# Optimization experiments

Hardware: AMD Instinct MI355X
Metric: run time of the kernel (lower is better)

The kernel has to match this reference:

```python
import jax, jax.numpy as jnp
import numpy as np
from jax import lax

SPARSITY = 0.5  # args.sparsity: fraction of weights KEPT


def get_subnet(scores, k):
    """GetSubnet.forward: sort |scores|, zero lowest (1-k) fraction, one elsewhere."""
    sa = jnp.abs(scores)
    n = sa.size
    j = int((1.0 - k) * n)  # static: number of entries zeroed
    idx = jnp.argsort(sa.ravel())  # ascending, matches torch .sort()
    mask = jnp.zeros((n,), dtype=sa.dtype).at[idx[j:]].set(1.0)
    return mask.reshape(scores.shape)


def masked_conv(x, w, s, b, stride):
    m = get_subnet(s, SPARSITY)
    y = lax.conv_general_dilated(
        x, w * m, window_strides=(stride, stride), padding=((1, 1), (1, 1)),
        dimension_numbers=('NCHW', 'OIHW', 'NCHW'))
    return y + b[None, :, None, None]


def setup_inputs() -> dict:
    key = jax.random.key(0)
    ks = jax.random.split(key, 16)
    def rn(k, shape, scale):
        return jax.random.normal(k, shape, dtype=jnp.float32) * scale
    return {
        'x':   rn(ks[0], (64, 3, 64, 64), 1.0),
        'w1':  rn(ks[1], (128, 3, 3, 3), 0.2),   's1': rn(ks[2], (128, 3, 3, 3), 1.0),   'b1': rn(ks[3], (128,), 0.01),
        'w2':  rn(ks[4], (256, 128, 3, 3), 0.05), 's2': rn(ks[5], (256, 128, 3, 3), 1.0), 'b2': rn(ks[6], (256,), 0.01),
        'w3':  rn(ks[7], (512, 256, 3, 3), 0.03), 's3': rn(ks[8], (512, 256, 3, 3), 1.0), 'b3': rn(ks[9], (512,), 0.01),
        'fw1': rn(ks[10], (1024, 512), 0.05),     'fs1': rn(ks[11], (1024, 512), 1.0),    'fb1': rn(ks[12], (1024,), 0.01),
        'fw2': rn(ks[13], (10, 1024), 0.05),      'fs2': rn(ks[14], (10, 1024), 1.0),     'fb2': rn(ks[15], (10,), 0.01),
    }


def reference(x, w1, s1, b1, w2, s2, b2, w3, s3, b3, fw1, fs1, fb1, fw2, fs2, fb2):
    h = jax.nn.relu(masked_conv(x, w1, s1, b1, stride=1))   # [64,128,64,64]
    h = jax.nn.relu(masked_conv(h, w2, s2, b2, stride=2))   # [64,256,32,32]
    h = jax.nn.relu(masked_conv(h, w3, s3, b3, stride=2))   # [64,512,16,16]
    h = h.mean(axis=(2, 3))                                 # [64,512] global avg pool
    m1 = get_subnet(fs1, SPARSITY)
    h = jax.nn.relu(h @ (fw1 * m1).T + fb1)                 # [64,1024]
    m2 = get_subnet(fs2, SPARSITY)
    return h @ (fw2 * m2).T + fb2                           # [64,10]
```

## Files before the change

### kernel.cpp

```cpp
#include <hip/hip_runtime.h>
#include <stdint.h>


typedef __attribute__((ext_vector_type(8))) short short8;
typedef __attribute__((ext_vector_type(4))) short short4v;
typedef __attribute__((ext_vector_type(4))) float floatx4;
typedef __attribute__((ext_vector_type(4))) int int4v;

__device__ __forceinline__ unsigned short f2bf(float f) {
    unsigned u = __float_as_uint(f);
    u += 0x7fffu + ((u >> 16) & 1u);
    return (unsigned short)(u >> 16);
}

__device__ __forceinline__ short8 gload16(const unsigned short* p) {
    int4v d;
    asm volatile("global_load_dwordx4 %0, %1, off" : "=v"(d) : "v"(p));
    union { int4v i; short8 s; } u;
    u.i = d;
    return u.s;
}

constexpr unsigned CUM0 = 3456u;
constexpr unsigned CUM1 = 298368u;
constexpr unsigned CUM2 = 1478016u;
constexpr unsigned CUM3 = 2002304u;
constexpr unsigned STOT = 2012544u;
constexpr int NBH = 512;

__device__ __forceinline__ int find_tensor(unsigned idx, unsigned& li) {
    if (idx < CUM0) { li = idx;        return 0; }
    if (idx < CUM1) { li = idx - CUM0; return 1; }
    if (idx < CUM2) { li = idx - CUM1; return 2; }
    if (idx < CUM3) { li = idx - CUM2; return 3; }
    li = idx - CUM3; return 4;
}

__global__ __launch_bounds__(256) void hist11(const float* __restrict__ s0,
                                              const float* __restrict__ s1,
                                              const float* __restrict__ s2,
                                              const float* __restrict__ s3,
                                              const float* __restrict__ s4,
                                              const unsigned* __restrict__ P,
                                              unsigned* __restrict__ ghist, int pass) {
    __shared__ unsigned lh[10240];
    const int tid = threadIdx.x;
    const int NB = (pass == 2) ? 512 : 2048;
    for (int i = tid; i < NB * 5; i += 256) lh[i] = 0;
    __syncthreads();

    unsigned pref[5];
    #pragma unroll
    for (int t = 0; t < 5; t++) pref[t] = pass ? P[t] : 0u;
    const int fsh = (pass == 1) ? 20 : 9;

    for (unsigned idx = blockIdx.x * 256u + tid; idx < STOT; idx += NBH * 256u) {
        unsigned li; int t = find_tensor(idx, li);
        const float* sp = t == 0 ? s0 : t == 1 ? s1 : t == 2 ? s2 : t == 3 ? s3 : s4;
        unsigned key = __float_as_uint(sp[li]) & 0x7fffffffu;
        bool ok = (pass == 0) || ((key >> fsh) == pref[t]);
        if (ok) {
            unsigned bin = (pass == 0) ? (key >> 20)
                         : (pass == 1) ? ((key >> 9) & 2047u)
                                       : (key & 511u);
            atomicAdd(&lh[(unsigned)t * NB + bin], 1u);
        }
    }
    __syncthreads();
    const int goff = (pass == 0) ? 0 : (pass == 1) ? 10240 : 20480;
    for (int i = tid; i < NB * 5; i += 256) {
        unsigned v = lh[i];
        if (v) atomicAdd(&ghist[goff + i], v);
    }
}

__global__ __launch_bounds__(256) void find11(const unsigned* __restrict__ ghist,
                                              unsigned* __restrict__ P,
                                              unsigned* __restrict__ targ, int pass) {
    const int t = blockIdx.x;
    const int tid = threadIdx.x;
    const int NB = (pass == 2) ? 512 : 2048;
    const int goff = (pass == 0) ? 0 : (pass == 1) ? 10240 : 20480;
    const int seg = NB / 256;
    __shared__ unsigned bins[2048];
    __shared__ unsigned part[256];
    for (int i = tid; i < NB; i += 256) bins[i] = ghist[goff + t * NB + i];
    __syncthreads();
    unsigned s = 0;
    for (int j = 0; j < seg; j++) s += bins[tid * seg + j];
    part[tid] = s;
    __syncthreads();
    if (tid == 0) {
        unsigned n = t == 0 ? 3456u : t == 1 ? 294912u : t == 2 ? 1179648u
                   : t == 3 ? 524288u : 10240u;
        unsigned target = (pass == 0) ? (n >> 1) : targ[t];
        unsigned cum = 0; int q = 0;
        for (; q < 256; q++) { unsigned c = part[q]; if (cum + c > target) break; cum += c; }
        int b = q * seg;
        for (;; b++) { unsigned c = bins[b]; if (cum + c > target) break; cum += c; }
        targ[t] = target - cum;
        if (pass == 0)      P[t] = (unsigned)b;
        else if (pass == 1) P[t] = (P[t] << 11) | (unsigned)b;
        else                P[t] = (P[t] << 9) | (unsigned)b;
    }
}

__global__ void mask_reorder(const float* __restrict__ w0, const float* __restrict__ w1,
                             const float* __restrict__ w2, const float* __restrict__ w3,
                             const float* __restrict__ w4,
                             const float* __restrict__ s0, const float* __restrict__ s1,
                             const float* __restrict__ s2, const float* __restrict__ s3,
                             const float* __restrict__ s4,
                             const unsigned* __restrict__ T,
                             float* __restrict__ wm1,
                             unsigned short* __restrict__ A2,
                             unsigned short* __restrict__ A3,
                             float* __restrict__ fwm1, float* __restrict__ fwm2,
                             float* __restrict__ pooled) {
    unsigned idx = blockIdx.x * 256u + threadIdx.x;
    if (idx >= STOT) return;
    if (idx < 32768u) pooled[idx] = 0.f;
    unsigned li; int t = find_tensor(idx, li);
    const float* sp = t == 0 ? s0 : t == 1 ? s1 : t == 2 ? s2 : t == 3 ? s3 : s4;
    const float* wp = t == 0 ? w0 : t == 1 ? w1 : t == 2 ? w2 : t == 3 ? w3 : w4;
    unsigned key = __float_as_uint(sp[li]) & 0x7fffffffu;
    float val = (key >= T[t]) ? wp[li] : 0.f;
    if (t == 0) {
        wm1[li] = val;
    } else if (t == 1) {
        unsigned k = li / 1152u, r = li - k * 1152u;
        unsigned c = r / 9u, e = r - c * 9u;
        A2[((size_t)e * 256u + k) * 128u + c] = f2bf(val);
    } else if (t == 2) {
        unsigned k = li / 2304u, r = li - k * 2304u;
        unsigned c = r / 9u, e = r - c * 9u;
        A3[((size_t)e * 512u + k) * 256u + c] = f2bf(val);
    } else if (t == 3) {
        fwm1[li] = val;
    } else {
        fwm2[li] = val;
    }
}

template <int C, int H, int W, int K, int TX, int TY, int KT>
__global__ __launch_bounds__(TX* TY) void conv_direct(const float* __restrict__ in,
                                                      const float* __restrict__ wm,
                                                      const float* __restrict__ bias,
                                                      unsigned short* __restrict__ out) {
    constexpr int TILW = TX * 2, TILH = TY * 2;
    constexpr int ITW = TILW + 2, ITH = TILH + 2;
    constexpr int NTHREADS = TX * TY;
    constexpr int NLOAD = (ITH * ITW + NTHREADS - 1) / NTHREADS;
    constexpr int KG = K / KT;

    __shared__ float sIn[ITH * ITW];
    __shared__ float sW[9 * KT];

    const int tid = threadIdx.x;
    const int tx = tid % TX, ty = tid / TX;
    const int kg = blockIdx.z % KG, n = blockIdx.z / KG;
    const int ox0 = blockIdx.x * TILW, oy0 = blockIdx.y * TILH;
    const int ix0 = ox0 - 1, iy0 = oy0 - 1;

    const float* inN = in + (size_t)n * C * H * W;
    const float* wkg = wm + (size_t)kg * KT * C * 9;

    int goff[NLOAD];
    #pragma unroll
    for (int i = 0; i < NLOAD; i++) {
        int idx = tid + i * NTHREADS;
        if (idx < ITH * ITW) {
            int r = idx / ITW, col = idx % ITW;
            int gy = iy0 + r, gx = ix0 + col;
            goff[i] = (gy >= 0 && gy < H && gx >= 0 && gx < W) ? (gy * W + gx) : -1;
        } else goff[i] = -2;
    }

    float acc[2][2][KT];
    #pragma unroll
    for (int py = 0; py < 2; py++)
        #pragma unroll
        for (int px = 0; px < 2; px++)
            #pragma unroll
            for (int j = 0; j < KT; j++) acc[py][px][j] = 0.f;

    for (int c = 0; c < C; c++) {
        const float* inC = inN + (size_t)c * H * W;
        #pragma unroll
        for (int i = 0; i < NLOAD; i++) {
            int g = goff[i];
            if (g >= -1) sIn[tid + i * NTHREADS] = (g >= 0) ? inC[g] : 0.f;
        }
        for (int i = tid; i < 9 * KT; i += NTHREADS) {
            int e = i / KT, j = i % KT;
            sW[i] = wkg[j * C * 9 + c * 9 + e];
        }
        __syncthreads();

        float vin[4][4];
        const float* base = &sIn[(ty * 2) * ITW + tx * 2];
        #pragma unroll
        for (int r = 0; r < 4; r++)
            #pragma unroll
            for (int cc = 0; cc < 4; cc++) vin[r][cc] = base[r * ITW + cc];

        #pragma unroll
        for (int e = 0; e < 9; e++) {
            const int dy = e / 3, dx = e % 3;
            #pragma unroll
            for (int j = 0; j < KT; j++) {
                float wv = sW[e * KT + j];
                #pragma unroll
                for (int py = 0; py < 2; py++)
                    #pragma unroll
                    for (int px = 0; px < 2; px++)
                        acc[py][px][j] = fmaf(vin[py + dy][px + dx], wv, acc[py][px][j]);
            }
        }
        __syncthreads();
    }

    float bj[KT];
    #pragma unroll
    for (int j = 0; j < KT; j++) bj[j] = bias[kg * KT + j];
    #pragma unroll
    for (int py = 0; py < 2; py++)
        #pragma unroll
        for (int px = 0; px < 2; px++) {
            int oy = oy0 + ty * 2 + py, ox = ox0 + tx * 2 + px;
            short8 v;
            #pragma unroll
            for (int j = 0; j < KT; j++) {
                float t = acc[py][px][j] + bj[j];
                v[j] = (short)f2bf(t > 0.f ? t : 0.f);
            }
            *(short8*)(out + ((size_t)(n * H + oy) * W + ox) * K + kg * KT) = v;
        }
}

template <int C, int H, int W, int KOUT, int NPIX, bool POOL, bool SWAPYZ>
__global__ __launch_bounds__(256, 3) void conv_mfma(const unsigned short* __restrict__ in,
                                                    const unsigned short* __restrict__ A,
                                                    const float* __restrict__ bias,
                                                    void* __restrict__ outv) {
    constexpr int OH = H / 2, OW = W / 2;
    constexpr int PR = NPIX / OW;
    constexpr int FN = NPIX / 16;
    constexpr int RH = 2 * PR + 1;
    constexpr int IW = W + 1;
    constexpr int NC = C / 32;
    constexpr int PSTR = 40;
    constexpr int NSLOT = RH * IW * 4;
    constexpr int SLMAX = (NSLOT + 255) / 256;

    __shared__ unsigned short sIn[RH * IW * PSTR];

    const int tid = threadIdx.x;
    const int lane = tid & 63;
    const int wv = tid >> 6;
    const int l15 = lane & 15;
    const int quad = lane >> 4;
    const int pt = blockIdx.x;
    const int kb = SWAPYZ ? blockIdx.z : blockIdx.y;
    const int n  = SWAPYZ ? blockIdx.y : blockIdx.z;
    const int k0 = kb * 128;
    const int oy0 = pt * PR;
    const int g0y = 2 * oy0 - 1;
    const int mw = wv * 32;

    int goff[SLMAX], slds[SLMAX];
    #pragma unroll
    for (int i = 0; i < SLMAX; i++) {
        int s = tid + i * 256;
        if (s < NSLOT) {
            int q = s & 3, pix = s >> 2;
            int ix = pix % IW, iy = pix / IW;
            int gy = g0y + iy, gx = ix - 1;
            slds[i] = pix * PSTR + q * 8;
            goff[i] = (gy >= 0 && gy < H && gx >= 0) ? ((gy * W + gx) * C + q * 8) : -1;
        } else { goff[i] = -2; slds[i] = 0; }
    }

    int pB[FN];
    #pragma unroll
    for (int fn = 0; fn < FN; fn++) {
        int p = fn * 16 + l15;
        int oyl = p / OW, oxl = p % OW;
        pB[fn] = (oyl * 2 * IW + oxl * 2) * PSTR + quad * 8;
    }

    const unsigned short* inN = in + (size_t)n * H * W * C;

    floatx4 acc[2][FN];
    #pragma unroll
    for (int fm = 0; fm < 2; fm++)
        #pragma unroll
        for (int fn = 0; fn < FN; fn++) acc[fm][fn] = (floatx4){0.f, 0.f, 0.f, 0.f};

    #pragma unroll 1
    for (int cc = 0; cc < NC; cc++) {
        const int cof = cc * 32;
        const unsigned short* Abase = A + (size_t)(k0 + mw + l15) * C + cof + quad * 8;
        const size_t estr = (size_t)KOUT * C;

        __syncthreads();

        short8 af[9][2];
        #pragma unroll
        for (int e = 0; e < 9; e++) {
            af[e][0] = gload16(Abase + (size_t)e * estr);
            af[e][1] = gload16(Abase + (size_t)e * estr + 16 * C);
        }

        #pragma unroll
        for (int i = 0; i < SLMAX; i++) {
            int g = goff[i];
            if (g >= 0) {
                *(short8*)&sIn[slds[i]] = *(const short8*)(inN + g + cof);
            } else if (g == -1 && cc == 0) {
                *(short8*)&sIn[slds[i]] = (short8){0, 0, 0, 0, 0, 0, 0, 0};
            }
        }
        __syncthreads();
        asm volatile("s_waitcnt vmcnt(0)" ::: "memory");
        __builtin_amdgcn_sched_barrier(0);

        #pragma unroll
        for (int e = 0; e < 9; e++) {
            const int dy = e / 3, dx = e - dy * 3;
            const int boff = (dy * IW + dx) * PSTR;
            short8 bfr[FN];
            #pragma unroll
            for (int fn = 0; fn < FN; fn++)
                bfr[fn] = *(const short8*)&sIn[pB[fn] + boff];
            #pragma unroll
            for (int fn = 0; fn < FN; fn++) {
                acc[0][fn] = __builtin_amdgcn_mfma_f32_16x16x32_bf16(af[e][0], bfr[fn], acc[0][fn], 0, 0, 0);
                acc[1][fn] = __builtin_amdgcn_mfma_f32_16x16x32_bf16(af[e][1], bfr[fn], acc[1][fn], 0, 0, 0);
            }
        }
    }

    if (!POOL) {
        unsigned short* out = (unsigned short*)outv;
        #pragma unroll
        for (int fm = 0; fm < 2; fm++) {
            const int k4 = k0 + mw + fm * 16 + quad * 4;
            float b0 = bias[k4], b1 = bias[k4 + 1], b2 = bias[k4 + 2], b3 = bias[k4 + 3];
            #pragma unroll
            for (int fn = 0; fn < FN; fn++) {
                int p = fn * 16 + l15;
                int oy = oy0 + p / OW, ox = p % OW;
                float v0 = acc[fm][fn][0] + b0, v1 = acc[fm][fn][1] + b1;
                float v2 = acc[fm][fn][2] + b2, v3 = acc[fm][fn][3] + b3;
                short4v v;
                v[0] = (short)f2bf(v0 > 0.f ? v0 : 0.f);
                v[1] = (short)f2bf(v1 > 0.f ? v1 : 0.f);
                v[2] = (short)f2bf(v2 > 0.f ? v2 : 0.f);
                v[3] = (short)f2bf(v3 > 0.f ? v3 : 0.f);
                *(short4v*)(out + ((size_t)(n * OH + oy) * OW + ox) * KOUT + k4) = v;
            }
        }
    } else {
        float* out = (float*)outv;
        #pragma unroll
        for (int fm = 0; fm < 2; fm++) {
            #pragma unroll
            for (int reg = 0; reg < 4; reg++) {
                int k = k0 + mw + fm * 16 + quad * 4 + reg;
                float bv = bias[k];
                float s = 0.f;
                #pragma unroll
                for (int fn = 0; fn < FN; fn++) {
                    float v = acc[fm][fn][reg] + bv;
                    s += v > 0.f ? v : 0.f;
                }
                s += __shfl_xor(s, 1); s += __shfl_xor(s, 2);
                s += __shfl_xor(s, 4); s += __shfl_xor(s, 8);
                if (l15 == 0) atomicAdd(&out[n * KOUT + k], s * (1.0f / (OH * OW)));
            }
        }
    }
}

__global__ void fc1_kernel(const float* __restrict__ pooled, const float* __restrict__ w,
                           const float* __restrict__ b, float* __restrict__ out) {
    int t = blockIdx.x * 256 + threadIdx.x;
    int o = t & 1023, n = t >> 10;
    const float4* w4 = (const float4*)(w + (size_t)o * 512);
    const float4* p4 = (const float4*)(pooled + (size_t)n * 512);
    float acc = 0.f;
    for (int i = 0; i < 128; i++) {
        float4 a = p4[i], ww = w4[i];
        acc += a.x * ww.x + a.y * ww.y + a.z * ww.z + a.w * ww.w;
    }
    acc += b[o];
    out[t] = acc > 0.f ? acc : 0.f;
}

__global__ void fc2_kernel(const float* __restrict__ h, const float* __restrict__ w,
                           const float* __restrict__ b, float* __restrict__ out) {
    int n = blockIdx.x, tid = threadIdx.x;
    __shared__ float redw[40];
    const float4* h4 = (const float4*)(h + (size_t)n * 1024);
    float4 a = h4[tid];
    for (int o = 0; o < 10; o++) {
        const float4* w4 = (const float4*)(w + (size_t)o * 1024);
        float4 ww = w4[tid];
        float v = a.x * ww.x + a.y * ww.y + a.z * ww.z + a.w * ww.w;
        for (int off = 32; off > 0; off >>= 1) v += __shfl_down(v, off);
        if ((tid & 63) == 0) redw[o * 4 + (tid >> 6)] = v;
    }
    __syncthreads();
    if (tid < 10) {
        float s = redw[tid * 4] + redw[tid * 4 + 1] + redw[tid * 4 + 2] + redw[tid * 4 + 3] + b[tid];
        out[n * 10 + tid] = s;
    }
}

extern "C" void kernel_launch(void* const* d_in, const int* in_sizes, int n_in,
                              void* d_out, int out_size, void* d_ws, size_t ws_size,
                              hipStream_t stream) {
    const float* x   = (const float*)d_in[0];
    const float* w1  = (const float*)d_in[1];
    const float* s1  = (const float*)d_in[2];
    const float* b1  = (const float*)d_in[3];
    const float* w2  = (const float*)d_in[4];
    const float* s2  = (const float*)d_in[5];
    const float* b2  = (const float*)d_in[6];
    const float* w3  = (const float*)d_in[7];
    const float* s3  = (const float*)d_in[8];
    const float* b3  = (const float*)d_in[9];
    const float* fw1 = (const float*)d_in[10];
    const float* fs1 = (const float*)d_in[11];
    const float* fb1 = (const float*)d_in[12];
    const float* fw2 = (const float*)d_in[13];
    const float* fs2 = (const float*)d_in[14];
    const float* fb2 = (const float*)d_in[15];
    float* out = (float*)d_out;

    char* ws = (char*)d_ws;
    size_t off = 0;
    auto alloc = [&](size_t bytes) -> char* {
        char* p = ws + off;
        off = (off + bytes + 255) & ~(size_t)255;
        return p;
    };
    unsigned* ghist = (unsigned*)alloc(23040ull * 4);
    unsigned* P     = (unsigned*)alloc(64);
    unsigned* targ  = (unsigned*)alloc(64);
    float* wm1  = (float*)alloc(3456ull * 4);
    float* fwm1 = (float*)alloc(524288ull * 4);
    float* fwm2 = (float*)alloc(10240ull * 4);
    unsigned short* A2 = (unsigned short*)alloc(294912ull * 2);
    unsigned short* A3 = (unsigned short*)alloc(1179648ull * 2);
    unsigned short* h1 = (unsigned short*)alloc(33554432ull * 2);
    unsigned short* h2 = (unsigned short*)alloc(16777216ull * 2);
    float* pooled = (float*)alloc(32768ull * 4);
    float* fc1h   = (float*)alloc(65536ull * 4);
    if (off > ws_size) return;

    (void)hipMemsetAsync(ghist, 0, 23040ull * 4, stream);

    for (int pass = 0; pass < 3; pass++) {
        hist11<<<NBH, 256, 0, stream>>>(s1, s2, s3, fs1, fs2, P, ghist, pass);
        find11<<<5, 256, 0, stream>>>(ghist, P, targ, pass);
    }
    int gs = (STOT + 255) / 256;
    mask_reorder<<<gs, 256, 0, stream>>>(w1, w2, w3, fw1, fw2, s1, s2, s3, fs1, fs2, P,
                                         wm1, A2, A3, fwm1, fwm2, pooled);

    conv_direct<3, 64, 64, 128, 16, 16, 8>
        <<<dim3(2, 2, 64 * 16), 256, 0, stream>>>(x, wm1, b1, h1);
    conv_mfma<128, 64, 64, 256, 64, false, false>
        <<<dim3(16, 2, 64), 256, 0, stream>>>(h1, A2, b2, h2);
    conv_mfma<256, 32, 32, 512, 64, true, true>
        <<<dim3(4, 64, 4), 256, 0, stream>>>(h2, A3, b3, pooled);

    fc1_kernel<<<256, 256, 0, stream>>>(pooled, fwm1, fb1, fc1h);
    fc2_kernel<<<64, 256, 0, stream>>>(fc1h, fwm2, fb2, out);
}
```

Baseline: 459.0 us.

## Double-buffer conv input staging via direct global-to-LDS loads with swizzled layout

Replaces the register-staged input tile copy in the MFMA conv kernels with global_load_lds direct-to-LDS loads into a double-buffered shared array, prefetching the next channel chunk while the current one is computed. The LDS layout changes from a padded per-pixel stride to a channel-quad-major layout with an XOR swizzle to avoid bank conflicts, and out-of-bounds pixels read from a zeroed guard buffer in the workspace. Weight fragment loads become plain loads instead of volatile asm. The cost is doubled LDS use, which may lower occupancy, and extra index arithmetic per LDS read.

```diff
diff --git a/kernel.cpp b/kernel.cpp
--- a/kernel.cpp
+++ b/kernel.cpp
@@ -5,7 +5,6 @@
 typedef __attribute__((ext_vector_type(8))) short short8;
 typedef __attribute__((ext_vector_type(4))) short short4v;
 typedef __attribute__((ext_vector_type(4))) float floatx4;
-typedef __attribute__((ext_vector_type(4))) int int4v;
 
 __device__ __forceinline__ unsigned short f2bf(float f) {
     unsigned u = __float_as_uint(f);
@@ -13,12 +12,11 @@
     return (unsigned short)(u >> 16);
 }
 
-__device__ __forceinline__ short8 gload16(const unsigned short* p) {
-    int4v d;
-    asm volatile("global_load_dwordx4 %0, %1, off" : "=v"(d) : "v"(p));
-    union { int4v i; short8 s; } u;
-    u.i = d;
-    return u.s;
+__device__ __forceinline__ void stage16(const unsigned short* g, unsigned short* l) {
+    __builtin_amdgcn_global_load_lds(
+        (const __attribute__((address_space(1))) unsigned int*)(const void*)g,
+        (__attribute__((address_space(3))) unsigned int*)(void*)l,
+        16, 0, 0);
 }
 
 constexpr unsigned CUM0 = 3456u;
@@ -242,6 +240,7 @@
 __global__ __launch_bounds__(256, 3) void conv_mfma(const unsigned short* __restrict__ in,
                                                     const unsigned short* __restrict__ A,
                                                     const float* __restrict__ bias,
+                                                    const unsigned short* __restrict__ zg,
                                                     void* __restrict__ outv) {
     constexpr int OH = H / 2, OW = W / 2;
     constexpr int PR = NPIX / OW;
@@ -249,11 +248,13 @@
     constexpr int RH = 2 * PR + 1;
     constexpr int IW = W + 1;
     constexpr int NC = C / 32;
-    constexpr int PSTR = 40;
-    constexpr int NSLOT = RH * IW * 4;
+    constexpr int NPT = RH * IW;
+    constexpr int NPTP = (NPT + 7) & ~7;
+    constexpr int NSLOT = 4 * NPTP;
     constexpr int SLMAX = (NSLOT + 255) / 256;
-
-    __shared__ unsigned short sIn[RH * IW * PSTR];
+    constexpr int SLOTS_PAD = SLMAX * 256;
+
+    __shared__ unsigned short sIn[2][SLOTS_PAD * 8];
 
     const int tid = threadIdx.x;
     const int lane = tid & 63;
@@ -268,25 +269,25 @@
     const int g0y = 2 * oy0 - 1;
     const int mw = wv * 32;
 
-    int goff[SLMAX], slds[SLMAX];
+    int goff[SLMAX];
     #pragma unroll
     for (int i = 0; i < SLMAX; i++) {
         int s = tid + i * 256;
-        if (s < NSLOT) {
-            int q = s & 3, pix = s >> 2;
-            int ix = pix % IW, iy = pix / IW;
-            int gy = g0y + iy, gx = ix - 1;
-            slds[i] = pix * PSTR + q * 8;
-            goff[i] = (gy >= 0 && gy < H && gx >= 0) ? ((gy * W + gx) * C + q * 8) : -1;
-        } else { goff[i] = -2; slds[i] = 0; }
-    }
-
-    int pB[FN];
+        int q = s / NPTP;
+        int pix = s - q * NPTP;
+        int pl = pix ^ ((pix >> 3) & 7);
+        int iy = pl / IW, ix = pl - iy * IW;
+        int gy = g0y + iy, gx = ix - 1;
+        bool ok = (q < 4) && (pl < NPT) && (gy >= 0) && (gy < H) && (gx >= 0);
+        goff[i] = ok ? ((gy * W + gx) * C + q * 8) : -1;
+    }
+
+    int pL[FN];
     #pragma unroll
     for (int fn = 0; fn < FN; fn++) {
         int p = fn * 16 + l15;
         int oyl = p / OW, oxl = p % OW;
-        pB[fn] = (oyl * 2 * IW + oxl * 2) * PSTR + quad * 8;
+        pL[fn] = oyl * 2 * IW + oxl * 2;
     }
 
     const unsigned short* inN = in + (size_t)n * H * W * C;
@@ -296,49 +297,60 @@
     for (int fm = 0; fm < 2; fm++)
         #pragma unroll
         for (int fn = 0; fn < FN; fn++) acc[fm][fn] = (floatx4){0.f, 0.f, 0.f, 0.f};
+
+    auto stage_chunk = [&](unsigned short* sbuf, int cc) {
+        const int cof = cc * 32;
+        #pragma unroll
+        for (int i = 0; i < SLMAX; i++) {
+            const unsigned short* src = (goff[i] >= 0) ? (inN + goff[i] + cof) : zg;
+            stage16(src, sbuf + (size_t)(tid + i * 256) * 8);
+        }
+    };
+
+    const size_t estr = (size_t)KOUT * C;
+
+    stage_chunk(&sIn[0][0], 0);
 
     #pragma unroll 1
     for (int cc = 0; cc < NC; cc++) {
-        const int cof = cc * 32;
-        const unsigned short* Abase = A + (size_t)(k0 + mw + l15) * C + cof + quad * 8;
-        const size_t estr = (size_t)KOUT * C;
-
-        __syncthreads();
-
+        const int cur = cc & 1;
+        const unsigned short* sb = &sIn[cur][0];
+
+        if (cc + 1 < NC) {
+            stage_chunk(&sIn[cur ^ 1][0], cc + 1);
+            asm volatile("s_waitcnt vmcnt(%0)" :: "n"(SLMAX) : "memory");
+        } else {
+            asm volatile("s_waitcnt vmcnt(0)" ::: "memory");
+        }
+        __builtin_amdgcn_s_barrier();
+        __builtin_amdgcn_sched_barrier(0);
+
+        const unsigned short* Abase = A + (size_t)(k0 + mw + l15) * C + cc * 32 + quad * 8;
         short8 af[9][2];
         #pragma unroll
         for (int e = 0; e < 9; e++) {
-            af[e][0] = gload16(Abase + (size_t)e * estr);
-            af[e][1] = gload16(Abase + (size_t)e * estr + 16 * C);
-        }
-
-        #pragma unroll
-        for (int i = 0; i < SLMAX; i++) {
-            int g = goff[i];
-            if (g >= 0) {
-                *(short8*)&sIn[slds[i]] = *(const short8*)(inN + g + cof);
-            } else if (g == -1 && cc == 0) {
-                *(short8*)&sIn[slds[i]] = (short8){0, 0, 0, 0, 0, 0, 0, 0};
-            }
-        }
-        __syncthreads();
-        asm volatile("s_waitcnt vmcnt(0)" ::: "memory");
-        __builtin_amdgcn_sched_barrier(0);
+            af[e][0] = *(const short8*)(Abase + (size_t)e * estr);
+            af[e][1] = *(const short8*)(Abase + (size_t)e * estr + 16 * C);
+        }
 
         #pragma unroll
         for (int e = 0; e < 9; e++) {
             const int dy = e / 3, dx = e - dy * 3;
-            const int boff = (dy * IW + dx) * PSTR;
+            const int tof = dy * IW + dx;
             short8 bfr[FN];
             #pragma unroll
-            for (int fn = 0; fn < FN; fn++)
-                bfr[fn] = *(const short8*)&sIn[pB[fn] + boff];
+            for (int fn = 0; fn < FN; fn++) {
+                int p = pL[fn] + tof;
+                int pl = p ^ ((p >> 3) & 7);
+                bfr[fn] = *(const short8*)(sb + ((size_t)quad * NPTP + pl) * 8);
+            }
             #pragma unroll
             for (int fn = 0; fn < FN; fn++) {
                 acc[0][fn] = __builtin_amdgcn_mfma_f32_16x16x32_bf16(af[e][0], bfr[fn], acc[0][fn], 0, 0, 0);
                 acc[1][fn] = __builtin_amdgcn_mfma_f32_16x16x32_bf16(af[e][1], bfr[fn], acc[1][fn], 0, 0, 0);
             }
         }
+        __builtin_amdgcn_s_barrier();
     }
 
     if (!POOL) {
@@ -447,6 +459,7 @@
         return p;
     };
     unsigned* ghist = (unsigned*)alloc(23040ull * 4);
+    unsigned short* zguard = (unsigned short*)alloc(256);
     unsigned* P     = (unsigned*)alloc(64);
     unsigned* targ  = (unsigned*)alloc(64);
     float* wm1  = (float*)alloc(3456ull * 4);
@@ -460,7 +473,7 @@
     float* fc1h   = (float*)alloc(65536ull * 4);
     if (off > ws_size) return;
 
-    (void)hipMemsetAsync(ghist, 0, 23040ull * 4, stream);
+    (void)hipMemsetAsync(ghist, 0, 23040ull * 4 + 256, stream);
 
     for (int pass = 0; pass < 3; pass++) {
         hist11<<<NBH, 256, 0, stream>>>(s1, s2, s3, fs1, fs2, P, ghist, pass);
@@ -473,9 +486,9 @@
     conv_direct<3, 64, 64, 128, 16, 16, 8>
         <<<dim3(2, 2, 64 * 16), 256, 0, stream>>>(x, wm1, b1, h1);
     conv_mfma<128, 64, 64, 256, 64, false, false>
-        <<<dim3(16, 2, 64), 256, 0, stream>>>(h1, A2, b2, h2);
+        <<<dim3(16, 2, 64), 256, 0, stream>>>(h1, A2, b2, zguard, h2);
     conv_mfma<256, 32, 32, 512, 64, true, true>
-        <<<dim3(4, 64, 4), 256, 0, stream>>>(h2, A3, b3, pooled);
+        <<<dim3(4, 64, 4), 256, 0, stream>>>(h2, A3, b3, zguard, pooled);
 
     fc1_kernel<<<256, 256, 0, stream>>>(pooled, fwm1, fb1, fc1h);
     fc2_kernel<<<64, 256, 0, stream>>>(fc1h, fwm2, fb2, out);
```

Measured after the change: 448.1 us. 1.02x faster.

## Read conv im2col operands directly from global memory instead of LDS staging

Applied to the files above, without the earlier changes.

The strided MFMA convolutions no longer stage the input tile in shared memory with barriers. Each lane now loads its B fragments straight from global memory, using a zeroed guard buffer for padded borders. Weight fragments are loaded per tap rather than all up front. The pixel tile per block doubles to 128, which halves the grid. The intent is to drop the LDS traffic and the syncthreads, and to rely on cache hits for the overlapping 3x3 windows. The costs are more global and cache load traffic, higher register pressure from the doubled accumulators, and fewer blocks to fill the GPU.

```diff
diff --git a/kernel.cpp b/kernel.cpp
--- a/kernel.cpp
+++ b/kernel.cpp
@@ -5,20 +5,11 @@
 typedef __attribute__((ext_vector_type(8))) short short8;
 typedef __attribute__((ext_vector_type(4))) short short4v;
 typedef __attribute__((ext_vector_type(4))) float floatx4;
-typedef __attribute__((ext_vector_type(4))) int int4v;
 
 __device__ __forceinline__ unsigned short f2bf(float f) {
     unsigned u = __float_as_uint(f);
     u += 0x7fffu + ((u >> 16) & 1u);
     return (unsigned short)(u >> 16);
-}
-
-__device__ __forceinline__ short8 gload16(const unsigned short* p) {
-    int4v d;
-    asm volatile("global_load_dwordx4 %0, %1, off" : "=v"(d) : "v"(p));
-    union { int4v i; short8 s; } u;
-    u.i = d;
-    return u.s;
 }
 
 constexpr unsigned CUM0 = 3456u;
@@ -238,22 +229,16 @@
         }
 }
 
-template <int C, int H, int W, int KOUT, int NPIX, bool POOL, bool SWAPYZ>
+template <int C, int H, int W, int KOUT, bool POOL, bool SWAPYZ>
 __global__ __launch_bounds__(256, 3) void conv_mfma(const unsigned short* __restrict__ in,
                                                     const unsigned short* __restrict__ A,
                                                     const float* __restrict__ bias,
+                                                    const unsigned short* __restrict__ zg,
                                                     void* __restrict__ outv) {
     constexpr int OH = H / 2, OW = W / 2;
-    constexpr int PR = NPIX / OW;
-    constexpr int FN = NPIX / 16;
-    constexpr int RH = 2 * PR + 1;
-    constexpr int IW = W + 1;
+    constexpr int PR = 128 / OW;
+    constexpr int FN = 8;
     constexpr int NC = C / 32;
-    constexpr int PSTR = 40;
-    constexpr int NSLOT = RH * IW * 4;
-    constexpr int SLMAX = (NSLOT + 255) / 256;
-
-    __shared__ unsigned short sIn[RH * IW * PSTR];
 
     const int tid = threadIdx.x;
     const int lane = tid & 63;
@@ -268,25 +253,17 @@
     const int g0y = 2 * oy0 - 1;
     const int mw = wv * 32;
 
-    int goff[SLMAX], slds[SLMAX];
-    #pragma unroll
-    for (int i = 0; i < SLMAX; i++) {
-        int s = tid + i * 256;
-        if (s < NSLOT) {
-            int q = s & 3, pix = s >> 2;
-            int ix = pix % IW, iy = pix / IW;
-            int gy = g0y + iy, gx = ix - 1;
-            slds[i] = pix * PSTR + q * 8;
-            goff[i] = (gy >= 0 && gy < H && gx >= 0) ? ((gy * W + gx) * C + q * 8) : -1;
-        } else { goff[i] = -2; slds[i] = 0; }
-    }
-
-    int pB[FN];
+    int bofs[FN];
+    bool rn[FN], cn[FN];
     #pragma unroll
     for (int fn = 0; fn < FN; fn++) {
         int p = fn * 16 + l15;
         int oyl = p / OW, oxl = p % OW;
-        pB[fn] = (oyl * 2 * IW + oxl * 2) * PSTR + quad * 8;
+        int gy = g0y + 2 * oyl;
+        int gx = 2 * oxl - 1;
+        rn[fn] = (gy < 0);
+        cn[fn] = (gx < 0);
+        bofs[fn] = (gy * W + gx) * C + quad * 8;
     }
 
     const unsigned short* inN = in + (size_t)n * H * W * C;
@@ -296,47 +273,36 @@
     for (int fm = 0; fm < 2; fm++)
         #pragma unroll
         for (int fn = 0; fn < FN; fn++) acc[fm][fn] = (floatx4){0.f, 0.f, 0.f, 0.f};
+
+    const size_t estr = (size_t)KOUT * C;
 
     #pragma unroll 1
     for (int cc = 0; cc < NC; cc++) {
         const int cof = cc * 32;
         const unsigned short* Abase = A + (size_t)(k0 + mw + l15) * C + cof + quad * 8;
-        const size_t estr = (size_t)KOUT * C;
-
-        __syncthreads();
-
-        short8 af[9][2];
-        #pragma unroll
-        for (int e = 0; e < 9; e++) {
-            af[e][0] = gload16(Abase + (size_t)e * estr);
-            af[e][1] = gload16(Abase + (size_t)e * estr + 16 * C);
-        }
-
-        #pragma unroll
-        for (int i = 0; i < SLMAX; i++) {
-            int g = goff[i];
-            if (g >= 0) {
-                *(short8*)&sIn[slds[i]] = *(const short8*)(inN + g + cof);
-            } else if (g == -1 && cc == 0) {
-                *(short8*)&sIn[slds[i]] = (short8){0, 0, 0, 0, 0, 0, 0, 0};
-            }
-        }
-        __syncthreads();
-        asm volatile("s_waitcnt vmcnt(0)" ::: "memory");
-        __builtin_amdgcn_sched_barrier(0);
 
         #pragma unroll
         for (int e = 0; e < 9; e++) {
             const int dy = e / 3, dx = e - dy * 3;
-            const int boff = (dy * IW + dx) * PSTR;
+            const int tof = (dy * W + dx) * C;
+
+            short8 a0 = *(const short8*)(Abase + (size_t)e * estr);
+            short8 a1 = *(const short8*)(Abase + (size_t)e * estr + 16 * C);
+
             short8 bfr[FN];
             #pragma unroll
-            for (int fn = 0; fn < FN; fn++)
-                bfr[fn] = *(const short8*)&sIn[pB[fn] + boff];
-            #pragma unroll
             for (int fn = 0; fn < FN; fn++) {
-                acc[0][fn] = __builtin_amdgcn_mfma_f32_16x16x32_bf16(af[e][0], bfr[fn], acc[0][fn], 0, 0, 0);
-                acc[1][fn] = __builtin_amdgcn_mfma_f32_16x16x32_bf16(af[e][1], bfr[fn], acc[1][fn], 0, 0, 0);
+                const unsigned short* p = inN + bofs[fn] + tof + cof;
+                if (dy == 0 || dx == 0) {
+                    bool bad = (dy == 0 && rn[fn]) || (dx == 0 && cn[fn]);
+                    p = bad ? zg : p;
+                }
+                bfr[fn] = *(const short8*)p;
+            }
+            #pragma unroll
+            for (int fn = 0; fn < FN; fn++) {
+                acc[0][fn] = __builtin_amdgcn_mfma_f32_16x16x32_bf16(a0, bfr[fn], acc[0][fn], 0, 0, 0);
+                acc[1][fn] = __builtin_amdgcn_mfma_f32_16x16x32_bf16(a1, bfr[fn], acc[1][fn], 0, 0, 0);
             }
         }
     }
@@ -447,6 +413,7 @@
         return p;
     };
     unsigned* ghist = (unsigned*)alloc(23040ull * 4);
+    unsigned short* zguard = (unsigned short*)alloc(256);
     unsigned* P     = (unsigned*)alloc(64);
     unsigned* targ  = (unsigned*)alloc(64);
     float* wm1  = (float*)alloc(3456ull * 4);
@@ -460,7 +427,7 @@
     float* fc1h   = (float*)alloc(65536ull * 4);
     if (off > ws_size) return;
 
-    (void)hipMemsetAsync(ghist, 0, 23040ull * 4, stream);
+    (void)hipMemsetAsync(ghist, 0, 23040ull * 4 + 256, stream);
 
     for (int pass = 0; pass < 3; pass++) {
         hist11<<<NBH, 256, 0, stream>>>(s1, s2, s3, fs1, fs2, P, ghist, pass);
@@ -472,10 +439,10 @@
 
     conv_direct<3, 64, 64, 128, 16, 16, 8>
         <<<dim3(2, 2, 64 * 16), 256, 0, stream>>>(x, wm1, b1, h1);
-    conv_mfma<128, 64, 64, 256, 64, false, false>
-        <<<dim3(16, 2, 64), 256, 0, stream>>>(h1, A2, b2, h2);
-    conv_mfma<256, 32, 32, 512, 64, true, true>
-        <<<dim3(4, 64, 4), 256, 0, stream>>>(h2, A3, b3, pooled);
+    conv_mfma<128, 64, 64, 256, false, false>
+        <<<dim3(8, 2, 64), 256, 0, stream>>>(h1, A2, b2, zguard, h2);
+    conv_mfma<256, 32, 32, 512, true, true>
+        <<<dim3(2, 64, 4), 256, 0, stream>>>(h2, A3, b3, zguard, pooled);
 
     fc1_kernel<<<256, 256, 0, stream>>>(pooled, fwm1, fb1, fc1h);
     fc2_kernel<<<64, 256, 0, stream>>>(fc1h, fwm2, fb2, out);
```

Result: slower. 594.4 us (+29.5%).
